# Optimization experiments

Measured on AMD Instinct MI355X. Metric: run time of the kernel, lower is better.

Reference implementation:

```python
import jax, jax.numpy as jnp
import numpy as np

B, S, D, H = 4, 512, 128, 8


def setup_inputs() -> dict:
    key = jax.random.key(0)
    k = jax.random.split(key, 5)
    # torch Linear(2D->D): weight [D, 2D]; we store transposed [2D, D] for x @ W
    w1 = jax.random.normal(k[0], (2 * D, D), jnp.float32) / np.sqrt(2 * D)
    b1 = jnp.zeros((D,), jnp.float32)
    w2 = jax.random.normal(k[1], (D, H), jnp.float32) / np.sqrt(D)
    b2 = jnp.zeros((H,), jnp.float32)
    node_features = jax.random.normal(k[2], (B, S, D), jnp.float32)
    return {"node_features": node_features, "w1": w1, "b1": b1, "w2": w2, "b2": b2}


def reference(node_features, w1, b1, w2, b2):
    # concat([x_i, x_j]) @ w1 == x_i @ w1[:D] + x_j @ w1[D:]  (exact same math,
    # avoids materializing the [B,S,S,2D] concatenated tensor)
    a = jnp.einsum('bsd,de->bse', node_features, w1[:D])   # row (i) projection
    c = jnp.einsum('bsd,de->bse', node_features, w1[D:])   # col (j) projection
    h = jax.nn.relu(a[:, :, None, :] + c[:, None, :, :] + b1)  # [B,S,S,D]
    e = jax.nn.sigmoid(jnp.einsum('bijd,dh->bijh', h, w2) + b2)  # [B,S,S,H]
    return jnp.transpose(e, (0, 3, 1, 2))  # [B,H,S,S]
```

## Files before the change

kernel.cpp:

```cpp
#include <hip/hip_runtime.h>
#include <hip/hip_bf16.h>

#define D_ 128
#define S_ 512
#define B_ 4
#define H_ 8

typedef short bf16x8 __attribute__((ext_vector_type(8)));
typedef float f32x4 __attribute__((ext_vector_type(4)));

__device__ __forceinline__ short f2bf(float f) {
  __hip_bfloat16 h = __float2bfloat16(f);
  return __builtin_bit_cast(short, h);
}
__device__ __forceinline__ float bf2f(short s) {
  unsigned u = ((unsigned)(unsigned short)s) << 16;
  return __builtin_bit_cast(float, u);
}
__device__ __forceinline__ float fsigmoid(float x) {
  return __builtin_amdgcn_rcpf(1.0f + __expf(-x));
}

__global__ __launch_bounds__(256)
void proj_kernel(const float* __restrict__ x, const float* __restrict__ w1,
                 const float* __restrict__ b1, float* __restrict__ Aq,
                 float* __restrict__ Cq) {
  __shared__ float xs[4 * D_];
  __shared__ f32x4 red[256][5];
  const int t = threadIdx.x;
  const int row0 = blockIdx.x * 4;
  ((float2*)xs)[t] = ((const float2*)(x + row0 * D_))[t];
  __syncthreads();
  const int combo = t & 63;
  const int e4 = (combo & 31) * 4;
  const int half = combo >> 5;
  const int kq = t >> 6;
  const float* w1p = w1 + (half * D_ + kq * 32) * D_ + e4;
  const float* xq = xs + kq * 32;
  f32x4 acc[4] = {};
  #pragma unroll 8
  for (int k = 0; k < 32; ++k) {
    float4 wv = *(const float4*)(w1p + k * D_);
    #pragma unroll
    for (int r = 0; r < 4; ++r) {
      float xv = xq[r * D_ + k];
      acc[r][0] += xv * wv.x; acc[r][1] += xv * wv.y;
      acc[r][2] += xv * wv.z; acc[r][3] += xv * wv.w;
    }
  }
  #pragma unroll
  for (int r = 0; r < 4; ++r) red[t][r] = acc[r];
  __syncthreads();
  const int r = t >> 6;
  const int c2 = t & 63;
  f32x4 s = red[c2][r];
  #pragma unroll
  for (int q = 1; q < 4; ++q) {
    f32x4 v = red[c2 + 64 * q][r];
    s[0] += v[0]; s[1] += v[1]; s[2] += v[2]; s[3] += v[3];
  }
  const int fe4 = (c2 & 31) * 4;
  const int row = row0 + r;
  if ((c2 >> 5) == 0) {
    float4 bv = *(const float4*)(b1 + fe4);
    s[0] += bv.x; s[1] += bv.y; s[2] += bv.z; s[3] += bv.w;
    *(f32x4*)(Aq + row * D_ + fe4) = s;
  } else {
    *(f32x4*)(Cq + row * D_ + fe4) = s;
  }
}

__global__ __launch_bounds__(512)
void edge_kernel(const float* __restrict__ Aq, const float* __restrict__ Cq,
                 const float* __restrict__ w2, const float* __restrict__ b2,
                 float* __restrict__ out) {
  __shared__ short cbf[S_ * D_];
  const int t = threadIdx.x;
  const int lane = t & 63;
  const int wid = t >> 6;
  const int b = blockIdx.x >> 6;
  const int i = (blockIdx.x & 63) * 8 + wid;

  {
    const float* cb = Cq + b * (S_ * D_);
    #pragma unroll 4
    for (int it = 0; it < 16; ++it) {
      int p = t + it * 512;
      int row = p >> 4;
      int u = p & 15;
      const float* src = cb + row * D_ + u * 8;
      float4 v0 = *(const float4*)src;
      float4 v1 = *(const float4*)(src + 4);
      bf16x8 w;
      w[0] = f2bf(v0.x); w[1] = f2bf(v0.y); w[2] = f2bf(v0.z); w[3] = f2bf(v0.w);
      w[4] = f2bf(v1.x); w[5] = f2bf(v1.y); w[6] = f2bf(v1.z); w[7] = f2bf(v1.w);
      int up = u ^ (row & 7);
      *(bf16x8*)(cbf + row * D_ + up * 8) = w;
    }
  }

  const int jcol = lane & 15;
  const int lgrp = lane >> 4;

  float areg[32];
  {
    const float* Ai = Aq + (b * S_ + i) * D_ + lgrp * 8;
    #pragma unroll
    for (int ch = 0; ch < 4; ++ch) {
      float4 v0 = *(const float4*)(Ai + ch * 32);
      float4 v1 = *(const float4*)(Ai + ch * 32 + 4);
      areg[ch*8+0] = v0.x; areg[ch*8+1] = v0.y;
      areg[ch*8+2] = v0.z; areg[ch*8+3] = v0.w;
      areg[ch*8+4] = v1.x; areg[ch*8+5] = v1.y;
      areg[ch*8+6] = v1.z; areg[ch*8+7] = v1.w;
    }
  }
  bf16x8 w2f[4];
  #pragma unroll
  for (int ch = 0; ch < 4; ++ch) {
    #pragma unroll
    for (int e = 0; e < 8; ++e) {
      float wv = (jcol < H_) ? w2[(ch * 32 + lgrp * 8 + e) * H_ + jcol] : 0.0f;
      w2f[ch][e] = f2bf(wv);
    }
  }
  const float b2v = (jcol < H_) ? b2[jcol] : 0.0f;
  float* outp = out + (((size_t)(b * H_ + (jcol & 7)) * S_ + i) * S_) + lgrp * 4;

  __syncthreads();

  for (int jt = 0; jt < 32; ++jt) {
    const int row = jt * 16 + jcol;
    const short* base = cbf + row * D_;
    const int sw = jcol & 7;
    f32x4 acc = {0.f, 0.f, 0.f, 0.f};
    #pragma unroll
    for (int ch = 0; ch < 4; ++ch) {
      int up = (ch * 4 + lgrp) ^ sw;
      bf16x8 cv = *(const bf16x8*)(base + up * 8);
      bf16x8 hf;
      #pragma unroll
      for (int e = 0; e < 8; ++e)
        hf[e] = f2bf(fmaxf(bf2f(cv[e]) + areg[ch*8+e], 0.f));
      acc = __builtin_amdgcn_mfma_f32_16x16x32_bf16(hf, w2f[ch], acc, 0, 0, 0);
    }
    if (jcol < H_) {
      float4 o;
      o.x = fsigmoid(acc[0] + b2v);
      o.y = fsigmoid(acc[1] + b2v);
      o.z = fsigmoid(acc[2] + b2v);
      o.w = fsigmoid(acc[3] + b2v);
      *(float4*)(outp + jt * 16) = o;
    }
  }
}

extern "C" void kernel_launch(void* const* d_in, const int* in_sizes, int n_in,
                              void* d_out, int out_size, void* d_ws, size_t ws_size,
                              hipStream_t stream) {
  const float* x  = (const float*)d_in[0];
  const float* w1 = (const float*)d_in[1];
  const float* b1 = (const float*)d_in[2];
  const float* w2 = (const float*)d_in[3];
  const float* b2 = (const float*)d_in[4];
  float* out = (float*)d_out;
  float* Aq = (float*)d_ws;
  float* Cq = Aq + B_ * S_ * D_;
  proj_kernel<<<(B_ * S_) / 4, 256, 0, stream>>>(x, w1, b1, Aq, Cq);
  edge_kernel<<<B_ * 64, 512, 0, stream>>>(Aq, Cq, w2, b2, out);
}
```

Baseline: 39.72 us.

## Split edge kernel over column halves and double-buffer LDS tile loads

The edge kernel's j dimension is split into two halves. This doubles the grid to 512 blocks and halves the LDS footprint per block to 64KB, so more blocks can be resident per CU. The inner loop now prefetches the next tile's LDS fragments into registers while computing the current one, and the add+relu uses packed float2 operations. The trade-off is that each block re-reads A rows and w2 twice and needs more registers for the double buffering, with launch bounds asking for 4 waves per SIMD.

```diff
diff --git a/kernel.cpp b/kernel.cpp
--- a/kernel.cpp
+++ b/kernel.cpp
@@ -8,6 +8,7 @@
 
 typedef short bf16x8 __attribute__((ext_vector_type(8)));
 typedef float f32x4 __attribute__((ext_vector_type(4)));
+typedef float f32x2 __attribute__((ext_vector_type(2)));
 
 __device__ __forceinline__ short f2bf(float f) {
   __hip_bfloat16 h = __float2bfloat16(f);
@@ -70,21 +71,23 @@
   }
 }
 
-__global__ __launch_bounds__(512)
+__global__ __launch_bounds__(512, 4)
 void edge_kernel(const float* __restrict__ Aq, const float* __restrict__ Cq,
                  const float* __restrict__ w2, const float* __restrict__ b2,
                  float* __restrict__ out) {
-  __shared__ short cbf[S_ * D_];
+  __shared__ short cbf[256 * D_];
   const int t = threadIdx.x;
   const int lane = t & 63;
   const int wid = t >> 6;
-  const int b = blockIdx.x >> 6;
-  const int i = (blockIdx.x & 63) * 8 + wid;
+  const int b  = blockIdx.x >> 7;
+  const int jh = (blockIdx.x >> 6) & 1;
+  const int ig = blockIdx.x & 63;
+  const int i = ig * 8 + wid;
 
   {
-    const float* cb = Cq + b * (S_ * D_);
-    #pragma unroll 4
-    for (int it = 0; it < 16; ++it) {
+    const float* cb = Cq + (b * S_ + jh * 256) * D_;
+    #pragma unroll
+    for (int it = 0; it < 8; ++it) {
       int p = t + it * 512;
       int row = p >> 4;
       int u = p & 15;
@@ -94,25 +97,25 @@
       bf16x8 w;
       w[0] = f2bf(v0.x); w[1] = f2bf(v0.y); w[2] = f2bf(v0.z); w[3] = f2bf(v0.w);
       w[4] = f2bf(v1.x); w[5] = f2bf(v1.y); w[6] = f2bf(v1.z); w[7] = f2bf(v1.w);
-      int up = u ^ (row & 7);
-      *(bf16x8*)(cbf + row * D_ + up * 8) = w;
+      *(bf16x8*)(cbf + row * D_ + (u ^ (row & 7)) * 8) = w;
     }
   }
 
   const int jcol = lane & 15;
   const int lgrp = lane >> 4;
+  const int sw = jcol & 7;
 
-  float areg[32];
+  f32x2 apk[4][4];
   {
     const float* Ai = Aq + (b * S_ + i) * D_ + lgrp * 8;
     #pragma unroll
     for (int ch = 0; ch < 4; ++ch) {
       float4 v0 = *(const float4*)(Ai + ch * 32);
       float4 v1 = *(const float4*)(Ai + ch * 32 + 4);
-      areg[ch*8+0] = v0.x; areg[ch*8+1] = v0.y;
-      areg[ch*8+2] = v0.z; areg[ch*8+3] = v0.w;
-      areg[ch*8+4] = v1.x; areg[ch*8+5] = v1.y;
-      areg[ch*8+6] = v1.z; areg[ch*8+7] = v1.w;
+      apk[ch][0][0] = v0.x; apk[ch][0][1] = v0.y;
+      apk[ch][1][0] = v0.z; apk[ch][1][1] = v0.w;
+      apk[ch][2][0] = v1.x; apk[ch][2][1] = v1.y;
+      apk[ch][3][0] = v1.z; apk[ch][3][1] = v1.w;
     }
   }
   bf16x8 w2f[4];
@@ -125,23 +128,32 @@
     }
   }
   const float b2v = (jcol < H_) ? b2[jcol] : 0.0f;
-  float* outp = out + (((size_t)(b * H_ + (jcol & 7)) * S_ + i) * S_) + lgrp * 4;
+  float* outp = out + (((size_t)(b * H_ + (jcol & 7)) * S_ + i) * S_)
+                + jh * 256 + lgrp * 4;
 
   __syncthreads();
 
-  for (int jt = 0; jt < 32; ++jt) {
-    const int row = jt * 16 + jcol;
-    const short* base = cbf + row * D_;
-    const int sw = jcol & 7;
+  bf16x8 cva[4], cvb[4];
+  auto LOADT = [&](bf16x8 (&dst)[4], int jt) {
+    const short* bp = cbf + (jt * 16 + jcol) * D_;
+    #pragma unroll
+    for (int ch = 0; ch < 4; ++ch)
+      dst[ch] = *(const bf16x8*)(bp + (((ch * 4 + lgrp) ^ sw) * 8));
+  };
+  auto COMPUTE = [&](bf16x8 (&cv)[4], int jt) {
     f32x4 acc = {0.f, 0.f, 0.f, 0.f};
     #pragma unroll
     for (int ch = 0; ch < 4; ++ch) {
-      int up = (ch * 4 + lgrp) ^ sw;
-      bf16x8 cv = *(const bf16x8*)(base + up * 8);
       bf16x8 hf;
       #pragma unroll
-      for (int e = 0; e < 8; ++e)
-        hf[e] = f2bf(fmaxf(bf2f(cv[e]) + areg[ch*8+e], 0.f));
+      for (int p = 0; p < 4; ++p) {
+        f32x2 v;
+        v[0] = bf2f(cv[ch][2 * p]);
+        v[1] = bf2f(cv[ch][2 * p + 1]);
+        v += apk[ch][p];
+        hf[2 * p]     = f2bf(fmaxf(v[0], 0.f));
+        hf[2 * p + 1] = f2bf(fmaxf(v[1], 0.f));
+      }
       acc = __builtin_amdgcn_mfma_f32_16x16x32_bf16(hf, w2f[ch], acc, 0, 0, 0);
     }
     if (jcol < H_) {
@@ -152,6 +164,15 @@
       o.w = fsigmoid(acc[3] + b2v);
       *(float4*)(outp + jt * 16) = o;
     }
+  };
+
+  LOADT(cva, 0);
+  #pragma unroll 1
+  for (int jt = 0; jt < 16; jt += 2) {
+    LOADT(cvb, jt + 1);
+    COMPUTE(cva, jt);
+    LOADT(cva, (jt + 2) & 15);
+    COMPUTE(cvb, jt + 1);
   }
 }
 
@@ -167,5 +188,5 @@
   float* Aq = (float*)d_ws;
   float* Cq = Aq + B_ * S_ * D_;
   proj_kernel<<<(B_ * S_) / 4, 256, 0, stream>>>(x, w1, b1, Aq, Cq);
-  edge_kernel<<<B_ * 64, 512, 0, stream>>>(Aq, Cq, w2, b2, out);
+  edge_kernel<<<B_ * 2 * 64, 512, 0, stream>>>(Aq, Cq, w2, b2, out);
 }
```

After: 37.85 us. 1.05x faster.
